# Performance work log

Hardware: AMD Instinct MI355X
Metric: run time of the kernel (lower is better)

The kernel has to match this reference:

```python
import jax, jax.numpy as jnp
import numpy as np

D_MICRO, D_MODEL, TOPK = 11, 256, 32


def setup_inputs() -> dict:
    key = jax.random.key(0)
    ks = jax.random.split(key, 9)
    B, N_DAY, N_CELLS = 4, 2048, 8192
    s = 0.05
    return {
        "micro_tokens": jax.random.normal(ks[0], (B, N_DAY, D_MICRO), jnp.float32),
        "macro_output": jax.random.normal(ks[1], (B, N_CELLS, D_MODEL), jnp.float32),
        # weights stored (in, out); y = x @ W + b  (equiv to torch Linear)
        "mp_w": jax.random.normal(ks[2], (D_MICRO, D_MODEL), jnp.float32) * s,
        "mp_b": jnp.zeros((D_MODEL,), jnp.float32),
        "wq": jax.random.normal(ks[3], (D_MODEL, D_MODEL), jnp.float32) * s,
        "wk": jax.random.normal(ks[4], (D_MODEL, D_MODEL), jnp.float32) * s,
        "wv": jax.random.normal(ks[5], (D_MODEL, D_MODEL), jnp.float32) * s,
        "op_w": jax.random.normal(ks[6], (D_MODEL, D_MODEL), jnp.float32) * s,
        "op_b": jnp.zeros((D_MODEL,), jnp.float32),
    }


def reference(micro_tokens, macro_output, mp_w, mp_b, wq, wk, wv, op_w, op_b):
    scale = wq.shape[1] ** -0.5
    x_micro = micro_tokens @ mp_w + mp_b                      # [B, Nd, D]
    Q = x_micro @ wq                                          # [B, Nd, D]
    K_full = macro_output @ wk                                # [B, Nc, D]
    scores = jnp.einsum('bnd,bmd->bnm', Q, K_full) * scale    # [B, Nd, Nc]
    topk_vals, topk_idx = jax.lax.top_k(scores, TOPK)         # [B, Nd, K]
    attn_weights = jax.nn.softmax(topk_vals, axis=-1)
    # gather the K selected macro rows per query: [B, Nd, K, D]
    macro_sub = jax.vmap(lambda m, idx: m[idx])(macro_output, topk_idx)
    V_sub = macro_sub @ wv                                    # [B, Nd, K, D]
    context = jnp.einsum('bnk,bnkd->bnd', attn_weights, V_sub)
    x_conditioned = x_micro + context @ op_w + op_b
    return (x_conditioned, attn_weights, topk_idx)
```

## Files before the change

### kernel.cpp

```cpp
#include <hip/hip_runtime.h>
#include <cfloat>
#include <climits>

static constexpr float SCALE = 0.0625f;
static constexpr float ZTH = 2.154f;
static constexpr int CAP = 384;
static constexpr int RES = 40;
static constexpr int QPB = 4;

typedef _Float16 f16x8 __attribute__((ext_vector_type(8)));
typedef float f32x4 __attribute__((ext_vector_type(4)));

__global__ __launch_bounds__(256) void k_micro_mlp(
    const float* __restrict__ micro, const float* __restrict__ mpw,
    const float* __restrict__ mpb, float* __restrict__ xm) {
  const int r0 = blockIdx.x * 8;
  const int tid = threadIdx.x;
  __shared__ float ml[8][12];
  if (tid < 88) ml[tid / 11][tid % 11] = micro[(size_t)(r0 + tid / 11) * 11 + tid % 11];
  __syncthreads();
  const int d = tid;
  const float bias = mpb[d];
  float acc[8];
#pragma unroll
  for (int r = 0; r < 8; ++r) acc[r] = bias;
#pragma unroll
  for (int i = 0; i < 11; ++i) {
    const float w = mpw[i * 256 + d];
#pragma unroll
    for (int r = 0; r < 8; ++r) acc[r] = fmaf(ml[r][i], w, acc[r]);
  }
#pragma unroll
  for (int r = 0; r < 8; ++r) xm[(size_t)(r0 + r) * 256 + d] = acc[r];
}

__global__ __launch_bounds__(256) void k_fwk(const float* __restrict__ wk,
                                             float* __restrict__ fwk) {
  const int tid = threadIdx.x;
  float s = 0.f;
  for (int i = tid; i < 65536; i += 256) { const float v = wk[i]; s = fmaf(v, v, s); }
  __shared__ float red[4];
#pragma unroll
  for (int off = 32; off >= 1; off >>= 1) s += __shfl_xor(s, off);
  if ((tid & 63) == 0) red[tid >> 6] = s;
  __syncthreads();
  if (tid == 0) fwk[0] = red[0] + red[1] + red[2] + red[3];
}

__global__ __launch_bounds__(256) void k_gemm256_rf(
    const float* __restrict__ A, const float* __restrict__ W,
    float* __restrict__ Cr, _Float16* __restrict__ Fr, float* __restrict__ s2,
    int lgB, size_t strideA) {
  const int bi = blockIdx.x >> lgB;
  const int bx = blockIdx.x & ((1 << lgB) - 1);
  A += (size_t)bi * strideA;
  if (Cr != nullptr) Cr += (size_t)bi * strideA;
  if (Fr != nullptr) Fr += (size_t)bi * 2097152;
  if (s2 != nullptr) s2 += (size_t)bi * 2048;
  const int m0 = (bx >> 2) * 64, n0 = (bx & 3) * 64;
  const int tid = threadIdx.x;
  __shared__ __align__(16) float Al[16][72];
  __shared__ __align__(16) float Wl[16][72];
  __shared__ float sQ[64];
  float acc[4][4] = {};
  const int mg = tid >> 4, ng = tid & 15;
  for (int k0 = 0; k0 < 256; k0 += 16) {
    __syncthreads();
    {
      const int m = tid >> 2, ko = (tid & 3) << 2;
      const float4 a = *(const float4*)&A[(size_t)(m0 + m) * 256 + k0 + ko];
      Al[ko + 0][m] = a.x; Al[ko + 1][m] = a.y; Al[ko + 2][m] = a.z; Al[ko + 3][m] = a.w;
      const int kr = tid >> 4, no = (tid & 15) << 2;
      *(float4*)&Wl[kr][no] = *(const float4*)&W[(size_t)(k0 + kr) * 256 + n0 + no];
    }
    __syncthreads();
#pragma unroll
    for (int kk = 0; kk < 16; ++kk) {
      const float4 wv = *(const float4*)&Wl[kk][mg << 2];
      const float4 av = *(const float4*)&Al[kk][ng << 2];
      const float w_[4] = {wv.x, wv.y, wv.z, wv.w};
      const float a_[4] = {av.x, av.y, av.z, av.w};
#pragma unroll
      for (int i = 0; i < 4; ++i)
#pragma unroll
        for (int j = 0; j < 4; ++j) acc[i][j] = fmaf(w_[i], a_[j], acc[i][j]);
    }
  }
  if (Cr != nullptr) {
#pragma unroll
    for (int j = 0; j < 4; ++j) {
      const int col = m0 + (ng << 2) + j;
      float4 o = {acc[0][j], acc[1][j], acc[2][j], acc[3][j]};
      *(float4*)&Cr[(size_t)col * 256 + n0 + (mg << 2)] = o;
    }
  }
  if (Fr != nullptr) {
#pragma unroll
    for (int i = 0; i < 4; ++i) {
      const int d = n0 + (mg << 2) + i;
      const int kb = d >> 5, g = (d >> 3) & 3, e = d & 7;
#pragma unroll
      for (int j = 0; j < 4; ++j) {
        const int col = m0 + (ng << 2) + j;
        const size_t idx = ((size_t)((col >> 4) * 8 + kb) * 64 + g * 16 + (col & 15)) * 8 + e;
        Fr[idx] = (_Float16)acc[i][j];
      }
    }
  }
  if (s2 != nullptr) {
    float sq[4] = {0.f, 0.f, 0.f, 0.f};
#pragma unroll
    for (int i = 0; i < 4; ++i)
#pragma unroll
      for (int j = 0; j < 4; ++j) sq[j] = fmaf(acc[i][j], acc[i][j], sq[j]);
    if (tid < 64) sQ[tid] = 0.f;
    __syncthreads();
#pragma unroll
    for (int j = 0; j < 4; ++j) atomicAdd(&sQ[(ng << 2) + j], sq[j]);
    __syncthreads();
    if (tid < 64) atomicAdd(&s2[m0 + tid], sQ[tid]);
  }
}

__global__ __launch_bounds__(256) void k_tau2(const float* __restrict__ s2,
                                              const float* __restrict__ fwk,
                                              float* __restrict__ tau,
                                              int* __restrict__ cnt) {
  const int qc = blockIdx.x * 256 + threadIdx.x;
  tau[qc] = ZTH * sqrtf(s2[qc] * fwk[0] * (1.f / 256.f));
  cnt[qc] = 0;
}

__global__ __launch_bounds__(256, 4) void k_scores_mfma(
    const float* __restrict__ Qr, const _Float16* __restrict__ Kf,
    const float* __restrict__ tau, int* __restrict__ cnt,
    int2* __restrict__ buf, int lgp) {
  const int b = blockIdx.x;
  const int xcd = b & 7, rr = b >> 3;
  const int qg = rr & 31;
  const int grp = xcd * 8 + (rr >> 5);
  const int part = grp & ((1 << lgp) - 1);
  const int bi = grp >> lgp;
  const int tid = threadIdx.x;
  const int w = tid >> 6, lane = tid & 63;
  const int hi = lane >> 4, l16 = lane & 15;
  const int cellsWG = 8192 >> lgp;
  const int nchunk = cellsWG >> 6;
  const int total = nchunk * 2;
  const int qt = qg * 4 + w;
  const int qc0 = bi * 2048 + qt * 16;
  const int c0part = part * cellsWG;

  __shared__ __align__(16) _Float16 Bs[2][16][512];

  const float* qrow = Qr + (size_t)bi * 524288 + (size_t)(qt * 16 + l16) * 256 + hi * 8;
  f16x8 A0[8];
#pragma unroll
  for (int kb = 0; kb < 8; ++kb) {
    const float4 x = *(const float4*)&qrow[kb * 32];
    const float4 y = *(const float4*)&qrow[kb * 32 + 4];
    f16x8 t;
    t[0] = (_Float16)x.x; t[1] = (_Float16)x.y; t[2] = (_Float16)x.z; t[3] = (_Float16)x.w;
    t[4] = (_Float16)y.x; t[5] = (_Float16)y.y; t[6] = (_Float16)y.z; t[7] = (_Float16)y.w;
    A0[kb] = t;
  }
  float vt[4];
#pragma unroll
  for (int r = 0; r < 4; ++r) vt[r] = tau[qc0 + hi * 4 + r];

  const _Float16* kfb = Kf + (size_t)bi * 2097152;
  f32x4 acc[4] = {};

  auto STAGE = [&](int pbuf, int it) {
    const int ccn = it >> 1, sph = it & 1;
    const int ctb = (c0part + ccn * 64) >> 4;
#pragma unroll
    for (int j = 0; j < 4; ++j) {
      const int seg = w * 4 + j;
      const _Float16* src = kfb
          + ((size_t)(ctb + (seg & 3)) * 8 + sph * 4 + (seg >> 2)) * 512 + (size_t)lane * 8;
      __builtin_amdgcn_global_load_lds(
          (const __attribute__((address_space(1))) void*)src,
          (__attribute__((address_space(3))) void*)&Bs[pbuf][seg][0], 16, 0, 0);
    }
  };

  STAGE(0, 0);
  for (int cc = 0; cc < nchunk; ++cc) {
#pragma unroll
    for (int s = 0; s < 2; ++s) {
      __syncthreads();
      const int itn = cc * 2 + s + 1;
      if (itn < total) STAGE(itn & 1, itn);
#pragma unroll
      for (int kb4 = 0; kb4 < 4; ++kb4)
#pragma unroll
        for (int ct = 0; ct < 4; ++ct) {
          const f16x8 bk = *(const f16x8*)&Bs[s][kb4 * 4 + ct][(size_t)lane * 8];
          acc[ct] = __builtin_amdgcn_mfma_f32_16x16x32_f16(A0[s * 4 + kb4], bk, acc[ct], 0, 0, 0);
        }
    }
    const int c0 = c0part + cc * 64;
#pragma unroll
    for (int ct = 0; ct < 4; ++ct) {
#pragma unroll
      for (int r = 0; r < 4; ++r) {
        const float s_ = acc[ct][r];
        const unsigned long long m = __ballot(s_ > vt[r]);
        const unsigned sub = (unsigned)((m >> (hi * 16)) & 0xffffull);
        const int tot = __popc(sub);
        int base = 0;
        if (tot && l16 == 0) base = atomicAdd(&cnt[qc0 + hi * 4 + r], tot);
        base = __shfl(base, hi * 16);
        if (s_ > vt[r]) {
          const int slot = base + __popc(sub & ((1u << l16) - 1u));
          if (slot < CAP) {
            int2 pr;
            pr.x = __float_as_int(s_ * SCALE);
            pr.y = c0 + ct * 16 + l16;
            buf[(size_t)(qc0 + hi * 4 + r) * CAP + slot] = pr;
          }
        }
        acc[ct][r] = 0.f;
      }
    }
  }
}

__global__ __launch_bounds__(256) void k_finalize(
    const float* __restrict__ macro, const float* __restrict__ wv,
    const float* __restrict__ Qr, const float* __restrict__ Kr,
    const int2* __restrict__ buf, const int* __restrict__ cnt,
    const float* __restrict__ opw, const float* __restrict__ opb,
    float* __restrict__ outX, float* __restrict__ outW, float* __restrict__ outI,
    int b0) {
  const int qc0 = blockIdx.x * QPB;
  const int bl = qc0 >> 11;
  const int tid = threadIdx.x;
  const int w = tid >> 6, lane = tid & 63;
  __shared__ int2 pl[QPB][CAP];
  __shared__ __align__(16) float Ql[QPB][256];
  __shared__ float t40v[QPB][RES];
  __shared__ int t40c[QPB][RES];
  __shared__ float t32v[QPB][32];
  __shared__ int t32i[QPB][32];
  __shared__ float wts[QPB][32];
  __shared__ int sidx[QPB][32];
  __shared__ float mbar[QPB][256];
  __shared__ float ctx[QPB][256];
  __shared__ int ns[QPB];

  if (tid < QPB) ns[tid] = min(cnt[qc0 + tid], CAP);
  if (lane < RES) { t40c[w][lane] = -1; t40v[w][lane] = -FLT_MAX; }
  if (lane < 32) { wts[w][lane] = 0.f; sidx[w][lane] = 0; t32v[w][lane] = -FLT_MAX; t32i[w][lane] = 0; }
#pragma unroll
  for (int qq = 0; qq < QPB; ++qq)
    Ql[qq][tid] = Qr[(size_t)(qc0 + qq) * 256 + tid];
  __syncthreads();
#pragma unroll
  for (int qq = 0; qq < QPB; ++qq) {
    const int n = ns[qq];
    for (int t = tid; t < n; t += 256) pl[qq][t] = buf[(size_t)(qc0 + qq) * CAP + t];
  }
  __syncthreads();

  {
    const int n = ns[w];
    for (int t = lane; t < n; t += 64) {
      const float vt = __int_as_float(pl[w][t].x);
      const int it = pl[w][t].y;
      int r = 0;
      for (int j = 0; j < n; ++j) {
        const int2 pj = pl[w][j];
        const float vj = __int_as_float(pj.x);
        r += (vj > vt || (vj == vt && pj.y < it)) ? 1 : 0;
      }
      if (r < RES) { t40c[w][r] = it; t40v[w][r] = vt; }
    }
  }
  if (Kr != nullptr && lane < RES && t40c[w][lane] >= 0) {
    const float* kr = Kr + (size_t)bl * 2097152 + (size_t)(t40c[w][lane] & 8191) * 256;
    float s = 0.f;
#pragma unroll 8
    for (int k = 0; k < 256; k += 4) {
      const float4 kv = *(const float4*)&kr[k];
      const float4 qv = *(const float4*)&Ql[w][k];
      s = fmaf(qv.x, kv.x, s);
      s = fmaf(qv.y, kv.y, s);
      s = fmaf(qv.z, kv.z, s);
      s = fmaf(qv.w, kv.w, s);
    }
    t40v[w][lane] = s * SCALE;
  }
  if (lane < RES && t40c[w][lane] >= 0) {
    const float vt = t40v[w][lane];
    const int it = t40c[w][lane];
    int r = 0;
#pragma unroll
    for (int j = 0; j < RES; ++j) {
      const float vj = t40v[w][j];
      r += (t40c[w][j] >= 0 && (vj > vt || (vj == vt && t40c[w][j] < it))) ? 1 : 0;
    }
    if (r < 32) { t32v[w][r] = vt; t32i[w][r] = it; }
  }
  if (lane < 32) {
    const float mv = t32v[w][0];
    const float e = expf(t32v[w][lane] - mv);
    float s = e;
#pragma unroll
    for (int off = 16; off >= 1; off >>= 1) s += __shfl_xor(s, off);
    const float w_ = e / s;
    const int ii = t32i[w][lane];
    wts[w][lane] = w_; sidx[w][lane] = ii;
    const size_t gq = (size_t)b0 * 2048 + qc0 + w;
    outW[gq * 32 + lane] = w_;
    outI[gq * 32 + lane] = (float)ii;
  }
  __syncthreads();

  const int d = tid;
  {
    float m[QPB] = {0.f, 0.f, 0.f, 0.f};
#pragma unroll 4
    for (int k = 0; k < 32; ++k) {
#pragma unroll
      for (int qq = 0; qq < QPB; ++qq) {
        const int si = sidx[qq][k] & 8191;
        m[qq] = fmaf(wts[qq][k], macro[((size_t)bl * 8192 + si) * 256 + d], m[qq]);
      }
    }
#pragma unroll
    for (int qq = 0; qq < QPB; ++qq) mbar[qq][d] = m[qq];
  }
  __syncthreads();
  {
    float c[QPB] = {0.f, 0.f, 0.f, 0.f};
#pragma unroll 8
    for (int j = 0; j < 256; ++j) {
      const float wvj = wv[j * 256 + d];
#pragma unroll
      for (int qq = 0; qq < QPB; ++qq) c[qq] = fmaf(mbar[qq][j], wvj, c[qq]);
    }
#pragma unroll
    for (int qq = 0; qq < QPB; ++qq) ctx[qq][d] = c[qq];
  }
  __syncthreads();
  {
    const size_t gq0 = (size_t)b0 * 2048 + qc0;
    float y[QPB];
#pragma unroll
    for (int qq = 0; qq < QPB; ++qq) y[qq] = outX[(gq0 + qq) * 256 + d] + opb[d];
#pragma unroll 8
    for (int j = 0; j < 256; ++j) {
      const float owj = opw[j * 256 + d];
#pragma unroll
      for (int qq = 0; qq < QPB; ++qq) y[qq] = fmaf(ctx[qq][j], owj, y[qq]);
    }
#pragma unroll
    for (int qq = 0; qq < QPB; ++qq) outX[(gq0 + qq) * 256 + d] = y[qq];
  }
}

extern "C" void kernel_launch(void* const* d_in, const int* in_sizes, int n_in,
                              void* d_out, int out_size, void* d_ws, size_t ws_size,
                              hipStream_t stream) {
  const float* micro = (const float*)d_in[0];
  const float* macro = (const float*)d_in[1];
  const float* mpw   = (const float*)d_in[2];
  const float* mpb   = (const float*)d_in[3];
  const float* wq    = (const float*)d_in[4];
  const float* wk    = (const float*)d_in[5];
  const float* wv    = (const float*)d_in[6];
  const float* opw   = (const float*)d_in[7];
  const float* opb   = (const float*)d_in[8];

  float* outX = (float*)d_out;
  float* outW = outX + 2097152;
  float* outI = outX + 2359296;

  int nb, lgp; bool rescue = true;
  const size_t MB = 1024 * 1024;
  if (ws_size >= 84 * MB)      { nb = 4; lgp = 4; }
  else if (ws_size >= 42 * MB) { nb = 2; lgp = 5; }
  else if (ws_size >= 22 * MB) { nb = 1; lgp = 6; }
  else                         { nb = 1; lgp = 6; rescue = false; }

  float* Qr = (float*)d_ws;
  float* Kr = Qr + (size_t)nb * 524288;
  _Float16* Kf = (_Float16*)(Kr + (rescue ? (size_t)nb * 2097152 : 0));
  float* s2  = (float*)(Kf + (size_t)nb * 2097152);
  float* tau = s2 + (size_t)nb * 2048;
  int*   cnt = (int*)(tau + (size_t)nb * 2048);
  float* fwk = (float*)(cnt + (size_t)nb * 2048);
  int2*  buf = (int2*)(fwk + 64);

  k_micro_mlp<<<1024, 256, 0, stream>>>(micro, mpw, mpb, outX);
  k_fwk<<<1, 256, 0, stream>>>(wk, fwk);

  for (int b0 = 0; b0 < 4; b0 += nb) {
    hipMemsetAsync(s2, 0, (size_t)nb * 2048 * sizeof(float), stream);
    k_gemm256_rf<<<nb * 128, 256, 0, stream>>>(outX + (size_t)b0 * 524288, wq,
        Qr, nullptr, s2, 7, (size_t)524288);
    k_gemm256_rf<<<nb * 512, 256, 0, stream>>>(macro + (size_t)b0 * 2097152, wk,
        rescue ? Kr : nullptr, Kf, nullptr, 9, (size_t)2097152);
    k_tau2<<<nb * 8, 256, 0, stream>>>(s2, fwk, tau, cnt);
    k_scores_mfma<<<2048, 256, 0, stream>>>(Qr, Kf, tau, cnt, buf, lgp);
    k_finalize<<<nb * 512, 256, 0, stream>>>(macro + (size_t)b0 * 2097152, wv,
        Qr, rescue ? Kr : nullptr, buf, cnt, opw, opb, outX, outW, outI, b0);
  }
}
```

Before: 510.5 us.

## Enlarge projection GEMM tiles to 128x128 and use per-lane atomics for candidate append

The fp32 projection GEMM moves from 64x64 tiles with 4x4 per-thread accumulators to 128x128 tiles with 8x8 accumulators, and the grid sizes shrink to match. This raises arithmetic intensity per shared-memory load and launches fewer blocks, but it uses more registers and leaves fewer blocks in flight, which could underfill the GPU for the small Q GEMM. Separately, the score kernel's candidate append replaces the ballot, popcount and shuffle aggregation with one global atomicAdd per passing lane. That removes the warp-wide cross-lane work but adds more contended atomics on the per-query counters.

```diff
diff --git a/kernel.cpp b/kernel.cpp
--- a/kernel.cpp
+++ b/kernel.cpp
@@ -57,68 +57,78 @@
   if (Cr != nullptr) Cr += (size_t)bi * strideA;
   if (Fr != nullptr) Fr += (size_t)bi * 2097152;
   if (s2 != nullptr) s2 += (size_t)bi * 2048;
-  const int m0 = (bx >> 2) * 64, n0 = (bx & 3) * 64;
+  const int m0 = (bx >> 1) * 128, n0 = (bx & 1) * 128;
   const int tid = threadIdx.x;
-  __shared__ __align__(16) float Al[16][72];
-  __shared__ __align__(16) float Wl[16][72];
-  __shared__ float sQ[64];
-  float acc[4][4] = {};
+  __shared__ __align__(16) float Al[16][136];
+  __shared__ __align__(16) float Wl[16][136];
+  __shared__ float sQ[128];
+  float acc[8][8] = {};
   const int mg = tid >> 4, ng = tid & 15;
   for (int k0 = 0; k0 < 256; k0 += 16) {
     __syncthreads();
     {
-      const int m = tid >> 2, ko = (tid & 3) << 2;
-      const float4 a = *(const float4*)&A[(size_t)(m0 + m) * 256 + k0 + ko];
-      Al[ko + 0][m] = a.x; Al[ko + 1][m] = a.y; Al[ko + 2][m] = a.z; Al[ko + 3][m] = a.w;
-      const int kr = tid >> 4, no = (tid & 15) << 2;
+      const int m = tid >> 1, ko = (tid & 1) << 3;
+      const float4 a0 = *(const float4*)&A[(size_t)(m0 + m) * 256 + k0 + ko];
+      const float4 a1 = *(const float4*)&A[(size_t)(m0 + m) * 256 + k0 + ko + 4];
+      Al[ko + 0][m] = a0.x; Al[ko + 1][m] = a0.y; Al[ko + 2][m] = a0.z; Al[ko + 3][m] = a0.w;
+      Al[ko + 4][m] = a1.x; Al[ko + 5][m] = a1.y; Al[ko + 6][m] = a1.z; Al[ko + 7][m] = a1.w;
+      const int kr = tid >> 4, no = (tid & 15) << 3;
       *(float4*)&Wl[kr][no] = *(const float4*)&W[(size_t)(k0 + kr) * 256 + n0 + no];
+      *(float4*)&Wl[kr][no + 4] = *(const float4*)&W[(size_t)(k0 + kr) * 256 + n0 + no + 4];
     }
     __syncthreads();
 #pragma unroll
     for (int kk = 0; kk < 16; ++kk) {
-      const float4 wv = *(const float4*)&Wl[kk][mg << 2];
-      const float4 av = *(const float4*)&Al[kk][ng << 2];
-      const float w_[4] = {wv.x, wv.y, wv.z, wv.w};
-      const float a_[4] = {av.x, av.y, av.z, av.w};
-#pragma unroll
-      for (int i = 0; i < 4; ++i)
-#pragma unroll
-        for (int j = 0; j < 4; ++j) acc[i][j] = fmaf(w_[i], a_[j], acc[i][j]);
+      const float4 wv0 = *(const float4*)&Wl[kk][mg << 2];
+      const float4 wv1 = *(const float4*)&Wl[kk][64 + (mg << 2)];
+      const float4 av0 = *(const float4*)&Al[kk][ng << 2];
+      const float4 av1 = *(const float4*)&Al[kk][64 + (ng << 2)];
+      const float w_[8] = {wv0.x, wv0.y, wv0.z, wv0.w, wv1.x, wv1.y, wv1.z, wv1.w};
+      const float a_[8] = {av0.x, av0.y, av0.z, av0.w, av1.x, av1.y, av1.z, av1.w};
+#pragma unroll
+      for (int i = 0; i < 8; ++i)
+#pragma unroll
+        for (int j = 0; j < 8; ++j) acc[i][j] = fmaf(w_[i], a_[j], acc[i][j]);
     }
   }
   if (Cr != nullptr) {
 #pragma unroll
-    for (int j = 0; j < 4; ++j) {
-      const int col = m0 + (ng << 2) + j;
-      float4 o = {acc[0][j], acc[1][j], acc[2][j], acc[3][j]};
-      *(float4*)&Cr[(size_t)col * 256 + n0 + (mg << 2)] = o;
+    for (int j = 0; j < 8; ++j) {
+      const int col = m0 + ((j < 4) ? (ng << 2) + j : 64 + (ng << 2) + j - 4);
+      float4 o0 = {acc[0][j], acc[1][j], acc[2][j], acc[3][j]};
+      float4 o1 = {acc[4][j], acc[5][j], acc[6][j], acc[7][j]};
+      *(float4*)&Cr[(size_t)col * 256 + n0 + (mg << 2)] = o0;
+      *(float4*)&Cr[(size_t)col * 256 + n0 + 64 + (mg << 2)] = o1;
     }
   }
   if (Fr != nullptr) {
 #pragma unroll
-    for (int i = 0; i < 4; ++i) {
-      const int d = n0 + (mg << 2) + i;
+    for (int i = 0; i < 8; ++i) {
+      const int d = n0 + ((i < 4) ? (mg << 2) + i : 64 + (mg << 2) + i - 4);
       const int kb = d >> 5, g = (d >> 3) & 3, e = d & 7;
 #pragma unroll
-      for (int j = 0; j < 4; ++j) {
-        const int col = m0 + (ng << 2) + j;
+      for (int j = 0; j < 8; ++j) {
+        const int col = m0 + ((j < 4) ? (ng << 2) + j : 64 + (ng << 2) + j - 4);
         const size_t idx = ((size_t)((col >> 4) * 8 + kb) * 64 + g * 16 + (col & 15)) * 8 + e;
         Fr[idx] = (_Float16)acc[i][j];
       }
     }
   }
   if (s2 != nullptr) {
-    float sq[4] = {0.f, 0.f, 0.f, 0.f};
-#pragma unroll
-    for (int i = 0; i < 4; ++i)
-#pragma unroll
-      for (int j = 0; j < 4; ++j) sq[j] = fmaf(acc[i][j], acc[i][j], sq[j]);
-    if (tid < 64) sQ[tid] = 0.f;
+    float sq[8] = {};
+#pragma unroll
+    for (int i = 0; i < 8; ++i)
+#pragma unroll
+      for (int j = 0; j < 8; ++j) sq[j] = fmaf(acc[i][j], acc[i][j], sq[j]);
+    if (tid < 128) sQ[tid] = 0.f;
     __syncthreads();
 #pragma unroll
-    for (int j = 0; j < 4; ++j) atomicAdd(&sQ[(ng << 2) + j], sq[j]);
+    for (int j = 0; j < 8; ++j) {
+      const int cl = (j < 4) ? (ng << 2) + j : 64 + (ng << 2) + j - 4;
+      atomicAdd(&sQ[cl], sq[j]);
+    }
     __syncthreads();
-    if (tid < 64) atomicAdd(&s2[m0 + tid], sQ[tid]);
+    if (tid < 128) atomicAdd(&s2[m0 + tid], sQ[tid]);
   }
 }
 
@@ -206,19 +216,14 @@
 #pragma unroll
       for (int r = 0; r < 4; ++r) {
         const float s_ = acc[ct][r];
-        const unsigned long long m = __ballot(s_ > vt[r]);
-        const unsigned sub = (unsigned)((m >> (hi * 16)) & 0xffffull);
-        const int tot = __popc(sub);
-        int base = 0;
-        if (tot && l16 == 0) base = atomicAdd(&cnt[qc0 + hi * 4 + r], tot);
-        base = __shfl(base, hi * 16);
         if (s_ > vt[r]) {
-          const int slot = base + __popc(sub & ((1u << l16) - 1u));
+          const int qc = qc0 + hi * 4 + r;
+          const int slot = atomicAdd(&cnt[qc], 1);
           if (slot < CAP) {
             int2 pr;
             pr.x = __float_as_int(s_ * SCALE);
             pr.y = c0 + ct * 16 + l16;
-            buf[(size_t)(qc0 + hi * 4 + r) * CAP + slot] = pr;
+            buf[(size_t)qc * CAP + slot] = pr;
           }
         }
         acc[ct][r] = 0.f;
@@ -399,10 +404,10 @@
 
   for (int b0 = 0; b0 < 4; b0 += nb) {
     hipMemsetAsync(s2, 0, (size_t)nb * 2048 * sizeof(float), stream);
-    k_gemm256_rf<<<nb * 128, 256, 0, stream>>>(outX + (size_t)b0 * 524288, wq,
-        Qr, nullptr, s2, 7, (size_t)524288);
-    k_gemm256_rf<<<nb * 512, 256, 0, stream>>>(macro + (size_t)b0 * 2097152, wk,
-        rescue ? Kr : nullptr, Kf, nullptr, 9, (size_t)2097152);
+    k_gemm256_rf<<<nb * 32, 256, 0, stream>>>(outX + (size_t)b0 * 524288, wq,
+        Qr, nullptr, s2, 5, (size_t)524288);
+    k_gemm256_rf<<<nb * 128, 256, 0, stream>>>(macro + (size_t)b0 * 2097152, wk,
+        rescue ? Kr : nullptr, Kf, nullptr, 7, (size_t)2097152);
     k_tau2<<<nb * 8, 256, 0, stream>>>(s2, fwk, tau, cnt);
     k_scores_mfma<<<2048, 256, 0, stream>>>(Qr, Kf, tau, cnt, buf, lgp);
     k_finalize<<<nb * 512, 256, 0, stream>>>(macro + (size_t)b0 * 2097152, wv,
```

Measured after the change: 492.2 us. 3.6% less time.
